# Kernel optimization log

Hardware: AMD Instinct MI355X
Metric: run time of the kernel (lower is better)

Reference implementation:

```python
import jax, jax.numpy as jnp
import numpy as np

B = 64            # graphs
N0 = 1024         # nodes per graph at level 0
DEG = 16          # avg degree
D = 128
NS = [1024, 820, 656, 525, 420, 336]  # ceil(0.8*n) cascade


def gcn(x, src, dst, valid, W, b, num_nodes):
    # x: [N,D]; src/dst: [E] int; valid: [E] float mask; W: [D,D]; b: [D]
    x = x @ W.T + b
    deg = jax.ops.segment_sum(valid, src, num_segments=num_nodes) + 1.0  # +1 self loop
    dis = jax.lax.rsqrt(deg)
    norm = dis[src] * dis[dst] * valid
    agg = jax.ops.segment_sum(norm[:, None] * x[src], dst, num_segments=num_nodes)
    return agg + (dis * dis)[:, None] * x  # self-loop term


def topk_pool(x, src, dst, valid, w, n, k):
    # PyG TopKPooling: score = tanh((x.w)/||w||); keep top ceil(ratio*n) per graph
    s = jnp.tanh((x @ w) / jnp.linalg.norm(w))
    _, idx = jax.lax.top_k(s.reshape(B, n), k)                    # [B,k] local ids
    perm = (idx + (jnp.arange(B) * n)[:, None]).reshape(-1)       # global ids
    xn = x[perm] * s[perm][:, None]
    new_id = jnp.full((B * n,), -1, jnp.int32).at[perm].set(jnp.arange(B * k, dtype=jnp.int32))
    ns_, nd_ = new_id[src], new_id[dst]
    v = valid * ((ns_ >= 0) & (nd_ >= 0)).astype(jnp.float32)
    return xn, jnp.maximum(ns_, 0), jnp.maximum(nd_, 0), v


def setup_inputs() -> dict:
    key = jax.random.key(0)
    ks = jax.random.split(key, 32)
    x = jax.random.normal(ks[0], (B * N0, D), jnp.float32)
    eg = N0 * DEG  # edges per graph
    local = jax.random.randint(ks[1], (2, B, eg), 0, N0, jnp.int32)
    edge_index = (local + (jnp.arange(B, dtype=jnp.int32) * N0)[None, :, None]).reshape(2, -1)
    batch = jnp.repeat(jnp.arange(B, dtype=jnp.int32), N0)
    sc = 1.0 / np.sqrt(D)
    inp = {"x": x, "edge_index": edge_index, "batch": batch}
    for i in range(1, 6):
        inp[f"c{i}w"] = jax.random.normal(ks[2 * i], (D, D), jnp.float32) * sc
        inp[f"c{i}b"] = jnp.zeros((D,), jnp.float32)
        inp[f"p{i}w"] = jax.random.normal(ks[2 * i + 1], (D,), jnp.float32) * sc
    inp["l1w"] = jax.random.normal(ks[20], (128, 256), jnp.float32) / np.sqrt(256)
    inp["l1b"] = jnp.zeros((128,), jnp.float32)
    inp["l2w"] = jax.random.normal(ks[21], (64, 128), jnp.float32) * sc
    inp["l2b"] = jnp.zeros((64,), jnp.float32)
    inp["l3w"] = jax.random.normal(ks[22], (2, 64), jnp.float32) / np.sqrt(64)
    inp["l3b"] = jnp.zeros((2,), jnp.float32)
    return inp


def reference(x, edge_index, batch,
              c1w, c1b, p1w, c2w, c2b, p2w, c3w, c3b, p3w,
              c4w, c4b, p4w, c5w, c5b, p5w,
              l1w, l1b, l2w, l2b, l3w, l3b):
    src, dst = edge_index[0], edge_index[1]
    valid = jnp.ones(src.shape, jnp.float32)
    layers = [(c1w, c1b, p1w), (c2w, c2b, p2w), (c3w, c3b, p3w),
              (c4w, c4b, p4w), (c5w, c5b, p5w)]
    reads = []
    for i, (cw, cb, pw) in enumerate(layers):
        n, k = NS[i], NS[i + 1]
        x = jax.nn.relu(gcn(x, src, dst, valid, cw, cb, B * n))
        x, src, dst, valid = topk_pool(x, src, dst, valid, pw, n, k)
        xk = x.reshape(B, k, D)
        reads.append(jnp.concatenate([xk.max(axis=1), xk.mean(axis=1)], axis=1))
    h = reads[0] + reads[1] + reads[2] + reads[3] + reads[4]   # [B,256]
    h = jax.nn.relu(h @ l1w.T + l1b)
    # dropout is identity in eval mode
    h = jax.nn.relu(h @ l2w.T + l2b)
    return jax.nn.log_softmax(h @ l3w.T + l3b, axis=-1)       # [B,2]
```

## Files before the change

kernel.cpp:

```cpp
#include <hip/hip_runtime.h>
#include <math.h>

#define NB 64
#define DIM 128
#define ETOT 1048576
#define EPG 16384
#define EPT 16
#define WRS 192
#define XRS 96

static const int NS_H[6] = {1024, 820, 656, 525, 420, 336};

__global__ __launch_bounds__(1024) void init_kernel(const int* __restrict__ ei,
                                  int* __restrict__ src, int* __restrict__ dst,
                                  int2* __restrict__ epack, int* __restrict__ eoff,
                                  int* __restrict__ cnt, float* __restrict__ dinv,
                                  float* __restrict__ invn, const float* __restrict__ pw0,
                                  float* __restrict__ hsum) {
    __shared__ int hs[1024], hc[1024], cur[1024];
    __shared__ float dv[1024];
    __shared__ float shf[128];
    __shared__ int wsum[16];
    int g = blockIdx.x, t = threadIdx.x;
    int lane = t & 63, wv = t >> 6;
    hs[t] = 0; hc[t] = 0;
    if (t < 256) hsum[g * 256 + t] = 0.f;
    __syncthreads();
    int b0 = g * EPG;
    int sr[EPT], dr[EPT];
#pragma unroll
    for (int q = 0; q < EPT; q++) {
        int e = b0 + q * 1024 + t;
        int s = ei[e], d = ei[ETOT + e];
        sr[q] = s; dr[q] = d;
        src[e] = s; dst[e] = d;
        atomicAdd(&hs[s & 1023], 1);
        atomicAdd(&hc[d & 1023], 1);
    }
    __syncthreads();
    int v = hc[t];
    dv[t] = rsqrtf((float)hs[t] + 1.0f);
    int s = v;
#pragma unroll
    for (int off = 1; off < 64; off <<= 1) {
        int u = __shfl_up(s, off, 64);
        if (lane >= off) s += u;
    }
    if (lane == 63) wsum[wv] = s;
    __syncthreads();
    if (wv == 0) {
        int ws = (lane < 16) ? wsum[lane] : 0;
#pragma unroll
        for (int off = 1; off < 16; off <<= 1) {
            int u = __shfl_up(ws, off, 64);
            if (lane >= off) ws += u;
        }
        if (lane < 16) wsum[lane] = ws;
    }
    __syncthreads();
    int excl = b0 + s + ((wv > 0) ? wsum[wv - 1] : 0) - v;
    eoff[g * 1024 + t] = excl;
    cnt[g * 1024 + t] = v;
    dinv[g * 1024 + t] = dv[t];
    cur[t] = excl;
    __syncthreads();
#pragma unroll
    for (int q = 0; q < EPT; q++) {
        int sl = sr[q] & 1023, dl = dr[q] & 1023;
        int pos = atomicAdd(&cur[dl], 1);
        epack[pos] = make_int2(sr[q], __float_as_int(dv[sl] * dv[dl]));
    }
    if (g == 0) {
        if (t < 128) shf[t] = pw0[t] * pw0[t];
        __syncthreads();
        for (int q = 64; q > 0; q >>= 1) {
            if (t < q) shf[t] += shf[t + q];
            __syncthreads();
        }
        if (t == 0) invn[0] = rsqrtf(shf[0]);
    }
}

__global__ __launch_bounds__(256) void linear_kernel(const float* __restrict__ x,
                              const float* __restrict__ W, const float* __restrict__ b,
                              float* __restrict__ y, int N) {
    __shared__ float Wt[32 * WRS];
    __shared__ float xT[32 * XRS];
    int tid = threadIdx.x;
    int base = blockIdx.x * 64;
    int nf = tid & 15;
    int u  = tid >> 4;
    float acc[4][8];
    {
        float bv[8];
#pragma unroll
        for (int f = 0; f < 8; f++) bv[f] = b[u * 8 + f];
#pragma unroll
        for (int i = 0; i < 4; i++)
#pragma unroll
            for (int f = 0; f < 8; f++) acc[i][f] = bv[f];
    }
    for (int kb = 0; kb < 4; kb++) {
        __syncthreads();
#pragma unroll
        for (int q = 0; q < 4; q++) {
            int i = q * 256 + tid;
            int dq = i >> 7;
            int r = i & 127;
            int s = (r >> 3) * 12 + (r & 7);
            float4 wv = *(const float4*)(W + r * 128 + kb * 32 + dq * 4);
            Wt[(dq * 4 + 0) * WRS + s] = wv.x;
            Wt[(dq * 4 + 1) * WRS + s] = wv.y;
            Wt[(dq * 4 + 2) * WRS + s] = wv.z;
            Wt[(dq * 4 + 3) * WRS + s] = wv.w;
        }
#pragma unroll
        for (int q = 0; q < 2; q++) {
            int i = q * 256 + tid;
            int dq = i >> 6;
            int r = i & 63;
            int s = (r >> 3) * 12 + (r & 7);
            float4 xv = *(const float4*)(x + (size_t)(base + r) * DIM + kb * 32 + dq * 4);
            xT[(dq * 4 + 0) * XRS + s] = xv.x;
            xT[(dq * 4 + 1) * XRS + s] = xv.y;
            xT[(dq * 4 + 2) * XRS + s] = xv.z;
            xT[(dq * 4 + 3) * XRS + s] = xv.w;
        }
        __syncthreads();
#pragma unroll 4
        for (int d = 0; d < 32; d++) {
            float4 xv = *(const float4*)&xT[d * XRS + (nf >> 1) * 12 + (nf & 1) * 4];
            float4 wa = *(const float4*)&Wt[d * WRS + u * 12];
            float4 wb = *(const float4*)&Wt[d * WRS + u * 12 + 4];
            float xs[4] = {xv.x, xv.y, xv.z, xv.w};
            float ws[8] = {wa.x, wa.y, wa.z, wa.w, wb.x, wb.y, wb.z, wb.w};
#pragma unroll
            for (int i = 0; i < 4; i++)
#pragma unroll
                for (int f = 0; f < 8; f++)
                    acc[i][f] += xs[i] * ws[f];
        }
    }
#pragma unroll
    for (int i = 0; i < 4; i++) {
        int nd = base + nf * 4 + i;
        float* yp = y + (size_t)nd * DIM + u * 8;
        *(float4*)(yp + 0) = make_float4(acc[i][0], acc[i][1], acc[i][2], acc[i][3]);
        *(float4*)(yp + 4) = make_float4(acc[i][4], acc[i][5], acc[i][6], acc[i][7]);
    }
}

__global__ void fused_agg_kernel(const float* __restrict__ xL, const int2* __restrict__ epack,
                                 const int* __restrict__ eoff, const int* __restrict__ cnt,
                                 const float* __restrict__ dinv,
                                 const float* __restrict__ pw, const float* __restrict__ invn,
                                 float* __restrict__ xA, float* __restrict__ score, int n) {
    int t = threadIdx.x;
    int g = blockIdx.x % NB;
    int chunk = blockIdx.x / NB;
    int ln = chunk * 8 + (t >> 5);
    if (ln >= n) return;
    int node = g * n + ln;
    int lane = t & 31;
    float dsn = dinv[node];
    float4 sv = ((const float4*)(xL + (size_t)node * DIM))[lane];
    float w0 = dsn * dsn;
    float4 a0 = make_float4(sv.x * w0, sv.y * w0, sv.z * w0, sv.w * w0);
    float4 a1 = make_float4(0.f, 0.f, 0.f, 0.f);
    float4 a2 = make_float4(0.f, 0.f, 0.f, 0.f);
    float4 a3 = make_float4(0.f, 0.f, 0.f, 0.f);
    int s0 = eoff[node], s1 = s0 + cnt[node];
    int j = s0;
    int2 e0, e1, e2, e3;
    if (j + 3 < s1) { e0 = epack[j]; e1 = epack[j + 1]; e2 = epack[j + 2]; e3 = epack[j + 3]; }
    for (; j + 7 < s1; j += 4) {
        int2 f0 = epack[j + 4], f1 = epack[j + 5], f2 = epack[j + 6], f3 = epack[j + 7];
        float4 x0 = ((const float4*)(xL + (size_t)e0.x * DIM))[lane];
        float4 x1 = ((const float4*)(xL + (size_t)e1.x * DIM))[lane];
        float4 x2 = ((const float4*)(xL + (size_t)e2.x * DIM))[lane];
        float4 x3 = ((const float4*)(xL + (size_t)e3.x * DIM))[lane];
        float n0 = __int_as_float(e0.y), n1 = __int_as_float(e1.y);
        float n2 = __int_as_float(e2.y), n3 = __int_as_float(e3.y);
        a0.x += n0 * x0.x; a0.y += n0 * x0.y; a0.z += n0 * x0.z; a0.w += n0 * x0.w;
        a1.x += n1 * x1.x; a1.y += n1 * x1.y; a1.z += n1 * x1.z; a1.w += n1 * x1.w;
        a2.x += n2 * x2.x; a2.y += n2 * x2.y; a2.z += n2 * x2.z; a2.w += n2 * x2.w;
        a3.x += n3 * x3.x; a3.y += n3 * x3.y; a3.z += n3 * x3.z; a3.w += n3 * x3.w;
        e0 = f0; e1 = f1; e2 = f2; e3 = f3;
    }
    if (j + 3 < s1) {
        float4 x0 = ((const float4*)(xL + (size_t)e0.x * DIM))[lane];
        float4 x1 = ((const float4*)(xL + (size_t)e1.x * DIM))[lane];
        float4 x2 = ((const float4*)(xL + (size_t)e2.x * DIM))[lane];
        float4 x3 = ((const float4*)(xL + (size_t)e3.x * DIM))[lane];
        float n0 = __int_as_float(e0.y), n1 = __int_as_float(e1.y);
        float n2 = __int_as_float(e2.y), n3 = __int_as_float(e3.y);
        a0.x += n0 * x0.x; a0.y += n0 * x0.y; a0.z += n0 * x0.z; a0.w += n0 * x0.w;
        a1.x += n1 * x1.x; a1.y += n1 * x1.y; a1.z += n1 * x1.z; a1.w += n1 * x1.w;
        a2.x += n2 * x2.x; a2.y += n2 * x2.y; a2.z += n2 * x2.z; a2.w += n2 * x2.w;
        a3.x += n3 * x3.x; a3.y += n3 * x3.y; a3.z += n3 * x3.z; a3.w += n3 * x3.w;
        j += 4;
    }
    for (; j < s1; j++) {
        int2 eq = epack[j];
        float nq = __int_as_float(eq.y);
        float4 xq = ((const float4*)(xL + (size_t)eq.x * DIM))[lane];
        a0.x += nq * xq.x; a0.y += nq * xq.y; a0.z += nq * xq.z; a0.w += nq * xq.w;
    }
    float4 acc = make_float4(fmaxf(a0.x + a1.x + a2.x + a3.x, 0.f),
                             fmaxf(a0.y + a1.y + a2.y + a3.y, 0.f),
                             fmaxf(a0.z + a1.z + a2.z + a3.z, 0.f),
                             fmaxf(a0.w + a1.w + a2.w + a3.w, 0.f));
    ((float4*)(xA + (size_t)node * DIM))[lane] = acc;
    float4 pv = ((const float4*)pw)[lane];
    float dot = acc.x * pv.x + acc.y * pv.y + acc.z * pv.z + acc.w * pv.w;
    for (int off = 16; off >= 1; off >>= 1) dot += __shfl_xor(dot, off, 32);
    if (lane == 0) score[node] = tanhf(dot * invn[0]);
}

__global__ __launch_bounds__(1024) void pool_kernel(const float* __restrict__ score,
                              const float* __restrict__ xA, float* __restrict__ xn,
                              float* __restrict__ h, int* __restrict__ src,
                              int* __restrict__ dst, int2* __restrict__ epack,
                              int* __restrict__ eoff, int* __restrict__ cnt,
                              float* __restrict__ dinv, const float* __restrict__ pwN,
                              float* __restrict__ invn, int n, int k, int last,
                              const float* __restrict__ l1w, const float* __restrict__ l1b,
                              const float* __restrict__ l2w, const float* __restrict__ l2b,
                              const float* __restrict__ l3w, const float* __restrict__ l3b,
                              float* __restrict__ out) {
    __shared__ float keyS[2][1024];
    __shared__ int idxS[2][1024];
    __shared__ int nid[1024];
    __shared__ float4 smax[32][33];
    __shared__ float4 ssum[32][33];
    __shared__ int hs[1024], hc[1024], cur[1024];
    __shared__ float dv[1024];
    __shared__ float shf[128];
    __shared__ int wsum[16];
    __shared__ float hr[256], h1[128], h2[64], lz[2];
    int g = blockIdx.x, t = threadIdx.x;
    int lane = t & 63, wv = t >> 6;
    int b0 = g * EPG, gn = g * n, gk = g * k;
    float k_r = (t < n) ? score[g * n + t] : -2.0f;
    int i_r = t;
    hs[t] = 0; hc[t] = 0;
    int se[EPT], de[EPT];
    if (!last) {
#pragma unroll
        for (int q = 0; q < EPT; q++) {
            int e = b0 + q * 1024 + t;
            se[q] = src[e];
            de[q] = dst[e];
        }
    }
    int par = 0;
    for (unsigned ksz = 2; ksz <= 1024; ksz <<= 1) {
        for (unsigned jj = ksz >> 1; jj > 0; jj >>= 1) {
            float kq; int iq;
            if (jj >= 64) {
                keyS[par][t] = k_r; idxS[par][t] = i_r;
                __syncthreads();
                kq = keyS[par][t ^ jj]; iq = idxS[par][t ^ jj];
                par ^= 1;
            } else {
                kq = __shfl_xor(k_r, (int)jj, 64);
                iq = __shfl_xor(i_r, (int)jj, 64);
            }
            bool mineFirst = (k_r > kq) || (k_r == kq && i_r < iq);
            bool up = ((t & ksz) == 0);
            bool iAmLower = ((t & jj) == 0);
            bool keepMine = (iAmLower == up) ? mineFirst : !mineFirst;
            if (!keepMine) { k_r = kq; i_r = iq; }
        }
    }
    keyS[0][t] = k_r; idxS[0][t] = i_r;
    nid[i_r] = (t < (unsigned)k) ? t : -1;
    __syncthreads();
    int lane4 = t & 31;
    int ch = t >> 5;
    float4 mx = make_float4(-INFINITY, -INFINITY, -INFINITY, -INFINITY);
    float4 sm = make_float4(0.f, 0.f, 0.f, 0.f);
    for (int j = ch; j < k; j += 32) {
        int row = idxS[0][j];
        float sval = keyS[0][j];
        float4 vv = ((const float4*)(xA + ((size_t)g * n + row) * DIM))[lane4];
        vv.x *= sval; vv.y *= sval; vv.z *= sval; vv.w *= sval;
        if (!last) ((float4*)(xn + ((size_t)g * k + j) * DIM))[lane4] = vv;
        mx.x = fmaxf(mx.x, vv.x); mx.y = fmaxf(mx.y, vv.y);
        mx.z = fmaxf(mx.z, vv.z); mx.w = fmaxf(mx.w, vv.w);
        sm.x += vv.x; sm.y += vv.y; sm.z += vv.z; sm.w += vv.w;
    }
    smax[ch][lane4] = mx;
    ssum[ch][lane4] = sm;
    __syncthreads();
    for (int s = 16; s >= 1; s >>= 1) {
        if (ch < s) {
            float4 a = smax[ch][lane4], bb = smax[ch + s][lane4];
            a.x = fmaxf(a.x, bb.x); a.y = fmaxf(a.y, bb.y);
            a.z = fmaxf(a.z, bb.z); a.w = fmaxf(a.w, bb.w);
            smax[ch][lane4] = a;
            float4 c = ssum[ch][lane4], d = ssum[ch + s][lane4];
            c.x += d.x; c.y += d.y; c.z += d.z; c.w += d.w;
            ssum[ch][lane4] = c;
        }
        __syncthreads();
    }
    if (ch == 0) {
        float4 m = smax[0][lane4];
        float4 s4 = ssum[0][lane4];
        float invk = 1.0f / (float)k;
        int f0 = lane4 * 4;
        if (!last) {
            float* hp = h + g * 256;
            hp[f0 + 0] += m.x; hp[f0 + 1] += m.y; hp[f0 + 2] += m.z; hp[f0 + 3] += m.w;
            hp[128 + f0 + 0] += s4.x * invk; hp[128 + f0 + 1] += s4.y * invk;
            hp[128 + f0 + 2] += s4.z * invk; hp[128 + f0 + 3] += s4.w * invk;
        } else {
            const float* hp = h + g * 256;
            hr[f0 + 0] = hp[f0 + 0] + m.x; hr[f0 + 1] = hp[f0 + 1] + m.y;
            hr[f0 + 2] = hp[f0 + 2] + m.z; hr[f0 + 3] = hp[f0 + 3] + m.w;
            hr[128 + f0 + 0] = hp[128 + f0 + 0] + s4.x * invk;
            hr[128 + f0 + 1] = hp[128 + f0 + 1] + s4.y * invk;
            hr[128 + f0 + 2] = hp[128 + f0 + 2] + s4.z * invk;
            hr[128 + f0 + 3] = hp[128 + f0 + 3] + s4.w * invk;
        }
    }
    if (last) {
        __syncthreads();
        if (t < 128) {
            float a1 = l1b[t];
            for (int d = 0; d < 256; d++) a1 += hr[d] * l1w[t * 256 + d];
            h1[t] = fmaxf(a1, 0.f);
        }
        __syncthreads();
        if (t < 64) {
            float a2 = l2b[t];
            for (int d = 0; d < 128; d++) a2 += h1[d] * l2w[t * 128 + d];
            h2[t] = fmaxf(a2, 0.f);
        }
        __syncthreads();
        if (t < 2) {
            float a3 = l3b[t];
            for (int d = 0; d < 64; d++) a3 += h2[d] * l3w[t * 64 + d];
            lz[t] = a3;
        }
        __syncthreads();
        if (t < 2) {
            float z0 = lz[0], z1 = lz[1];
            float m = fmaxf(z0, z1);
            float lse = m + logf(expf(z0 - m) + expf(z1 - m));
            out[g * 2 + t] = lz[t] - lse;
        }
        return;
    }
    int sr[EPT], dr[EPT];
#pragma unroll
    for (int q = 0; q < EPT; q++) {
        int e = b0 + q * 1024 + t;
        int s = se[q];
        int s2 = -1, d2 = -1;
        if (s >= 0) {
            s2 = nid[s - gn];
            d2 = nid[de[q] - gn];
            if (s2 >= 0 && d2 >= 0) {
                src[e] = gk + s2;
                dst[e] = gk + d2;
                atomicAdd(&hs[s2], 1);
                atomicAdd(&hc[d2], 1);
            } else {
                src[e] = -1;
                dst[e] = -1;
                s2 = -1;
            }
        }
        sr[q] = s2; dr[q] = d2;
    }
    __syncthreads();
    int v = (t < k) ? hc[t] : 0;
    if (t < k) dv[t] = rsqrtf((float)hs[t] + 1.0f);
    int s = v;
#pragma unroll
    for (int off = 1; off < 64; off <<= 1) {
        int u = __shfl_up(s, off, 64);
        if (lane >= off) s += u;
    }
    if (lane == 63) wsum[wv] = s;
    __syncthreads();
    if (wv == 0) {
        int ws = (lane < 16) ? wsum[lane] : 0;
#pragma unroll
        for (int off = 1; off < 16; off <<= 1) {
            int u = __shfl_up(ws, off, 64);
            if (lane >= off) ws += u;
        }
        if (lane < 16) wsum[lane] = ws;
    }
    __syncthreads();
    if (t < k) {
        int excl = b0 + s + ((wv > 0) ? wsum[wv - 1] : 0) - v;
        eoff[gk + t] = excl;
        cnt[gk + t] = v;
        dinv[gk + t] = dv[t];
        cur[t] = excl;
    }
    __syncthreads();
#pragma unroll
    for (int q = 0; q < EPT; q++) {
        if (sr[q] >= 0) {
            int pos = atomicAdd(&cur[dr[q]], 1);
            epack[pos] = make_int2(gk + sr[q], __float_as_int(dv[sr[q]] * dv[dr[q]]));
        }
    }
    if (g == 0) {
        if (t < 128) shf[t] = pwN[t] * pwN[t];
        __syncthreads();
        for (int q = 64; q > 0; q >>= 1) {
            if (t < q) shf[t] += shf[t + q];
            __syncthreads();
        }
        if (t == 0) invn[0] = rsqrtf(shf[0]);
    }
}

extern "C" void kernel_launch(void* const* d_in, const int* in_sizes, int n_in,
                              void* d_out, int out_size, void* d_ws, size_t ws_size,
                              hipStream_t stream) {
    const float* x_in = (const float*)d_in[0];
    const int* edge_index = (const int*)d_in[1];
    const float *cw[5], *cb[5], *pw[5];
    for (int i = 0; i < 5; i++) {
        cw[i] = (const float*)d_in[3 + 3 * i];
        cb[i] = (const float*)d_in[4 + 3 * i];
        pw[i] = (const float*)d_in[5 + 3 * i];
    }
    const float* l1w = (const float*)d_in[18];
    const float* l1b = (const float*)d_in[19];
    const float* l2w = (const float*)d_in[20];
    const float* l2b = (const float*)d_in[21];
    const float* l3w = (const float*)d_in[22];
    const float* l3b = (const float*)d_in[23];
    float* out = (float*)d_out;

    char* w = (char*)d_ws;
    float* xA    = (float*)w; w += (size_t)65536 * DIM * 4;
    float* xB    = (float*)w; w += (size_t)65536 * DIM * 4;
    float* xL    = (float*)w; w += (size_t)65536 * DIM * 4;
    int*   src   = (int*)w;   w += (size_t)ETOT * 4;
    int*   dst   = (int*)w;   w += (size_t)ETOT * 4;
    int2*  epack = (int2*)w;  w += (size_t)ETOT * 8;
    int*   cnt   = (int*)w;   w += (size_t)65536 * 4;
    int*   eoff  = (int*)w;   w += (size_t)65536 * 4;
    float* dinv  = (float*)w; w += (size_t)65536 * 4;
    float* score = (float*)w; w += (size_t)65536 * 4;
    float* hsum  = (float*)w; w += (size_t)NB * 256 * 4;
    float* invn  = (float*)w; w += 4;

    init_kernel<<<NB, 1024, 0, stream>>>(edge_index, src, dst, epack, eoff, cnt, dinv,
                                         invn, pw[0], hsum);

    const float* xin = x_in;
    for (int i = 0; i < 5; i++) {
        int n = NS_H[i], k = NS_H[i + 1];
        int N = NB * n;

        linear_kernel<<<N / 64, 256, 0, stream>>>(xin, cw[i], cb[i], xL, N);
        int gpb = (n + 7) / 8;
        fused_agg_kernel<<<NB * gpb, 256, 0, stream>>>(xL, epack, eoff, cnt, dinv, pw[i],
                                                       invn, xA, score, n);
        pool_kernel<<<NB, 1024, 0, stream>>>(score, xA, xB, hsum, src, dst, epack, eoff,
                                             cnt, dinv, (i < 4) ? pw[i + 1] : pw[i], invn,
                                             n, k, (i == 4) ? 1 : 0,
                                             l1w, l1b, l2w, l2b, l3w, l3b, out);

        xin = xB;
    }
}
```

Before: 535.8 us.

## Merge layer-0 linear into init kernel and use nontemporal gather loads

The first GCN linear transform now runs as extra blocks inside the init kernel, so the edge preprocessing and the layer-0 matmul execute concurrently in one launch instead of two serialized ones. The new linear path uses a 128-node tile with 1024 threads and a transposed, padded LDS layout. Separately, the neighbor feature gathers in the aggregation kernel switch to nontemporal loads to reduce cache pollution. The risk is that nontemporal hints hurt reuse of gathered rows, since node features are read by many edges, and that the large shared-memory footprint limits occupancy of the merged kernel.

```diff
diff --git a/kernel.cpp b/kernel.cpp
--- a/kernel.cpp
+++ b/kernel.cpp
@@ -8,21 +8,92 @@
 #define EPT 16
 #define WRS 192
 #define XRS 96
+#define LIN0_BLOCKS 512
 
 static const int NS_H[6] = {1024, 820, 656, 525, 420, 336};
 
-__global__ __launch_bounds__(1024) void init_kernel(const int* __restrict__ ei,
+typedef float __attribute__((ext_vector_type(4))) f4v;
+__device__ __forceinline__ float4 ldnt4(const float* p) {
+    f4v v = __builtin_nontemporal_load((const f4v*)p);
+    return make_float4(v.x, v.y, v.z, v.w);
+}
+
+__global__ __launch_bounds__(1024) void init_linear_kernel(const float* __restrict__ x,
+                                  const float* __restrict__ W, const float* __restrict__ bb,
+                                  float* __restrict__ y, int N,
+                                  const int* __restrict__ ei,
                                   int* __restrict__ src, int* __restrict__ dst,
                                   int2* __restrict__ epack, int* __restrict__ eoff,
                                   int* __restrict__ cnt, float* __restrict__ dinv,
                                   float* __restrict__ invn, const float* __restrict__ pw0,
                                   float* __restrict__ hsum) {
-    __shared__ int hs[1024], hc[1024], cur[1024];
-    __shared__ float dv[1024];
-    __shared__ float shf[128];
-    __shared__ int wsum[16];
-    int g = blockIdx.x, t = threadIdx.x;
-    int lane = t & 63, wv = t >> 6;
+    __shared__ alignas(16) char LB[49152];
+    const int t = threadIdx.x;
+    if (blockIdx.x < LIN0_BLOCKS) {
+        float* Wt = (float*)(LB);
+        float* xT = (float*)(LB + 24576);
+        const int base = blockIdx.x << 7;
+        const int nf = t & 31;
+        const int u = t >> 5;
+        float acc[4][4];
+        {
+            float bv[4];
+#pragma unroll
+            for (int f = 0; f < 4; f++) bv[f] = bb[u * 4 + f];
+#pragma unroll
+            for (int i = 0; i < 4; i++)
+#pragma unroll
+                for (int f = 0; f < 4; f++) acc[i][f] = bv[f];
+        }
+        for (int kb = 0; kb < 4; kb++) {
+            __syncthreads();
+            {
+                const int dq = t >> 7;
+                const int r = t & 127;
+                const int sl = (r >> 3) * 12 + (r & 7);
+                float4 w4 = *(const float4*)(W + r * 128 + kb * 32 + dq * 4);
+                Wt[(dq * 4 + 0) * 192 + sl] = w4.x;
+                Wt[(dq * 4 + 1) * 192 + sl] = w4.y;
+                Wt[(dq * 4 + 2) * 192 + sl] = w4.z;
+                Wt[(dq * 4 + 3) * 192 + sl] = w4.w;
+                const int nd = base + r;
+                float4 x4 = (nd < N) ? *(const float4*)(x + (size_t)nd * DIM + kb * 32 + dq * 4)
+                                     : make_float4(0.f, 0.f, 0.f, 0.f);
+                xT[(dq * 4 + 0) * 192 + sl] = x4.x;
+                xT[(dq * 4 + 1) * 192 + sl] = x4.y;
+                xT[(dq * 4 + 2) * 192 + sl] = x4.z;
+                xT[(dq * 4 + 3) * 192 + sl] = x4.w;
+            }
+            __syncthreads();
+#pragma unroll 4
+            for (int d = 0; d < 32; d++) {
+                float4 xv = *(const float4*)&xT[d * 192 + (nf >> 1) * 12 + (nf & 1) * 4];
+                float4 wq = *(const float4*)&Wt[d * 192 + (u >> 1) * 12 + (u & 1) * 4];
+                float xs[4] = {xv.x, xv.y, xv.z, xv.w};
+                float ws[4] = {wq.x, wq.y, wq.z, wq.w};
+#pragma unroll
+                for (int i = 0; i < 4; i++)
+#pragma unroll
+                    for (int f = 0; f < 4; f++) acc[i][f] += xs[i] * ws[f];
+            }
+        }
+#pragma unroll
+        for (int i = 0; i < 4; i++) {
+            const int nd = base + nf * 4 + i;
+            if (nd < N)
+                *(float4*)(y + (size_t)nd * DIM + u * 4) =
+                    make_float4(acc[i][0], acc[i][1], acc[i][2], acc[i][3]);
+        }
+        return;
+    }
+    int* hs = (int*)(LB);
+    int* hc = (int*)(LB + 4096);
+    int* cur = (int*)(LB + 8192);
+    float* dv = (float*)(LB + 12288);
+    float* shf = (float*)(LB + 16384);
+    int* wsum = (int*)(LB + 16896);
+    const int g = blockIdx.x - LIN0_BLOCKS;
+    const int lane = t & 63, wv = t >> 6;
     hs[t] = 0; hc[t] = 0;
     if (t < 256) hsum[g * 256 + t] = 0.f;
     __syncthreads();
@@ -175,10 +246,10 @@
     if (j + 3 < s1) { e0 = epack[j]; e1 = epack[j + 1]; e2 = epack[j + 2]; e3 = epack[j + 3]; }
     for (; j + 7 < s1; j += 4) {
         int2 f0 = epack[j + 4], f1 = epack[j + 5], f2 = epack[j + 6], f3 = epack[j + 7];
-        float4 x0 = ((const float4*)(xL + (size_t)e0.x * DIM))[lane];
-        float4 x1 = ((const float4*)(xL + (size_t)e1.x * DIM))[lane];
-        float4 x2 = ((const float4*)(xL + (size_t)e2.x * DIM))[lane];
-        float4 x3 = ((const float4*)(xL + (size_t)e3.x * DIM))[lane];
+        float4 x0 = ldnt4(xL + (size_t)e0.x * DIM + lane * 4);
+        float4 x1 = ldnt4(xL + (size_t)e1.x * DIM + lane * 4);
+        float4 x2 = ldnt4(xL + (size_t)e2.x * DIM + lane * 4);
+        float4 x3 = ldnt4(xL + (size_t)e3.x * DIM + lane * 4);
         float n0 = __int_as_float(e0.y), n1 = __int_as_float(e1.y);
         float n2 = __int_as_float(e2.y), n3 = __int_as_float(e3.y);
         a0.x += n0 * x0.x; a0.y += n0 * x0.y; a0.z += n0 * x0.z; a0.w += n0 * x0.w;
@@ -188,10 +259,10 @@
         e0 = f0; e1 = f1; e2 = f2; e3 = f3;
     }
     if (j + 3 < s1) {
-        float4 x0 = ((const float4*)(xL + (size_t)e0.x * DIM))[lane];
-        float4 x1 = ((const float4*)(xL + (size_t)e1.x * DIM))[lane];
-        float4 x2 = ((const float4*)(xL + (size_t)e2.x * DIM))[lane];
-        float4 x3 = ((const float4*)(xL + (size_t)e3.x * DIM))[lane];
+        float4 x0 = ldnt4(xL + (size_t)e0.x * DIM + lane * 4);
+        float4 x1 = ldnt4(xL + (size_t)e1.x * DIM + lane * 4);
+        float4 x2 = ldnt4(xL + (size_t)e2.x * DIM + lane * 4);
+        float4 x3 = ldnt4(xL + (size_t)e3.x * DIM + lane * 4);
         float n0 = __int_as_float(e0.y), n1 = __int_as_float(e1.y);
         float n2 = __int_as_float(e2.y), n3 = __int_as_float(e3.y);
         a0.x += n0 * x0.x; a0.y += n0 * x0.y; a0.z += n0 * x0.z; a0.w += n0 * x0.w;
@@ -203,7 +274,7 @@
     for (; j < s1; j++) {
         int2 eq = epack[j];
         float nq = __int_as_float(eq.y);
-        float4 xq = ((const float4*)(xL + (size_t)eq.x * DIM))[lane];
+        float4 xq = ldnt4(xL + (size_t)eq.x * DIM + lane * 4);
         a0.x += nq * xq.x; a0.y += nq * xq.y; a0.z += nq * xq.z; a0.w += nq * xq.w;
     }
     float4 acc = make_float4(fmaxf(a0.x + a1.x + a2.x + a3.x, 0.f),
@@ -455,15 +526,17 @@
     float* hsum  = (float*)w; w += (size_t)NB * 256 * 4;
     float* invn  = (float*)w; w += 4;
 
-    init_kernel<<<NB, 1024, 0, stream>>>(edge_index, src, dst, epack, eoff, cnt, dinv,
-                                         invn, pw[0], hsum);
+    init_linear_kernel<<<LIN0_BLOCKS + NB, 1024, 0, stream>>>(
+        x_in, cw[0], cb[0], xL, NB * 1024,
+        edge_index, src, dst, epack, eoff, cnt, dinv, invn, pw[0], hsum);
 
     const float* xin = x_in;
     for (int i = 0; i < 5; i++) {
         int n = NS_H[i], k = NS_H[i + 1];
         int N = NB * n;
 
-        linear_kernel<<<N / 64, 256, 0, stream>>>(xin, cw[i], cb[i], xL, N);
+        if (i > 0)
+            linear_kernel<<<N / 64, 256, 0, stream>>>(xin, cw[i], cb[i], xL, N);
         int gpb = (n + 7) / 8;
         fused_agg_kernel<<<NB * gpb, 256, 0, stream>>>(xL, epack, eoff, cnt, dinv, pw[i],
                                                        invn, xA, score, n);
```

Result: slower. 589.6 us (+10.1%).
